# Kernel tuning notes

Measured on AMD Instinct MI355X. Metric: run time of the kernel, lower is better.

## Reference

```python
import jax, jax.numpy as jnp
import numpy as np

B, C, H, W = 8, 128, 256, 256

def setup_inputs() -> dict:
    key = jax.random.key(0)
    k1, k2 = jax.random.split(key)
    inp = jax.random.normal(k1, (B, C, H, W), dtype=jnp.float32)
    # learned per-channel convection vector (kaiming-uniform-ish small values)
    c = jax.random.normal(k2, (C, 2), dtype=jnp.float32) * 2.0
    return {"input": inp, "c": c}

def reference(input, c):
    """Per-channel translation (convection) of a [B,C,H,W] grid by vector c[ch] = (cy, cx),
    via separable bilinear interpolation with zero padding outside the domain:
    out[b,ch,h,w] = input_interp[b, ch, h - c[ch,0], w - c[ch,1]].
    """
    Bs, Cs, Hs, Ws = input.shape

    # ---- interpolate along H ----
    pos_y = jnp.arange(Hs, dtype=c.dtype)[None, :] - c[:, 0][:, None]   # [C,H]
    y0f = jnp.floor(pos_y)
    wy = pos_y - y0f                                                     # frac weight [C,H]
    y0 = y0f.astype(jnp.int32)
    y1 = y0 + 1

    def gather_h(idx):  # idx [C,H] -> [B,C,H,W], zero outside
        valid = ((idx >= 0) & (idx < Hs)).astype(input.dtype)
        idxc = jnp.clip(idx, 0, Hs - 1)
        g = jnp.take_along_axis(input, idxc[None, :, :, None], axis=2)
        return g * valid[None, :, :, None]

    xh = gather_h(y0) * (1.0 - wy)[None, :, :, None] + gather_h(y1) * wy[None, :, :, None]

    # ---- interpolate along W ----
    pos_x = jnp.arange(Ws, dtype=c.dtype)[None, :] - c[:, 1][:, None]   # [C,W]
    x0f = jnp.floor(pos_x)
    wx = pos_x - x0f                                                     # [C,W]
    x0 = x0f.astype(jnp.int32)
    x1 = x0 + 1

    def gather_w(idx):  # idx [C,W] -> [B,C,H,W], zero outside
        valid = ((idx >= 0) & (idx < Ws)).astype(input.dtype)
        idxc = jnp.clip(idx, 0, Ws - 1)
        g = jnp.take_along_axis(xh, idxc[None, :, None, :], axis=3)
        return g * valid[None, :, None, :]

    out = gather_w(x0) * (1.0 - wx)[None, :, None, :] + gather_w(x1) * wx[None, :, None, :]
    return out
```

## Files before the change

### kernel.cpp

```cpp
#include <hip/hip_runtime.h>

constexpr int Cn = 128, Hn = 256, Wn = 256;

__global__ __launch_bounds__(256) void convection_kernel(
    const float* __restrict__ in, const float* __restrict__ cvec, float* __restrict__ out)
{
    const int lane  = threadIdx.x & 63;
    const int wave  = (int)blockIdx.x * 4 + (threadIdx.x >> 6);
    const int plane = wave >> 3;
    const int h0    = (wave & 7) << 5;
    const int ch    = plane & (Cn - 1);

    const float cy = cvec[2 * ch];
    const float cx = cvec[2 * ch + 1];
    const float* __restrict__ pin = in  + ((long long)plane << 16);
    float* __restrict__ pout      = out + ((long long)plane << 16);

    const float ncx = fminf(fmaxf(-cx, -600.f), 600.f);
    const int D = (int)floorf(ncx);
    const int s = D >> 2;
    const int r = D & 3;
    int q0 = lane + s;     q0 = q0 < 0 ? 0 : (q0 > 63 ? 63 : q0);
    int q1 = lane + s + 1; q1 = q1 < 0 ? 0 : (q1 > 63 ? 63 : q1);

    float fx0[4], fx1[4];
    #pragma unroll
    for (int j = 0; j < 4; ++j) {
        const int   col  = 4 * lane + j;
        const float posx = (float)col - cx;
        const int   e0   = col + D;
        const float wx   = posx - (float)e0;
        fx0[j] = ((unsigned)e0       < (unsigned)Wn) ? (1.0f - wx) : 0.0f;
        fx1[j] = ((unsigned)(e0 + 1) < (unsigned)Wn) ? wx          : 0.0f;
    }

    auto mkwin = [&](const float4 g, float* w) {
        const float u0 = __shfl(g.x, q0), u1 = __shfl(g.y, q0),
                    u2 = __shfl(g.z, q0), u3 = __shfl(g.w, q0);
        const float u4 = __shfl(g.x, q1), u5 = __shfl(g.y, q1),
                    u6 = __shfl(g.z, q1), u7 = __shfl(g.w, q1);
        switch (r) {
            case 0:  w[0]=u0; w[1]=u1; w[2]=u2; w[3]=u3; w[4]=u4; break;
            case 1:  w[0]=u1; w[1]=u2; w[2]=u3; w[3]=u4; w[4]=u5; break;
            case 2:  w[0]=u2; w[1]=u3; w[2]=u4; w[3]=u5; w[4]=u6; break;
            default: w[0]=u3; w[1]=u4; w[2]=u5; w[3]=u6; w[4]=u7; break;
        }
    };
    auto y0of = [&](int h) -> int {
        const float p = (float)h - cy;
        const float f = floorf(p);
        return (int)fminf(fmaxf(f, -600.f), 600.f);
    };

    int y0c = y0of(h0);
    const int rA = min(max(y0c,     0), 255);
    const int rB = min(max(y0c + 1, 0), 255);
    const float4 A = *(const float4*)(pin + (rA << 8) + 4 * lane);
    const float4 B = *(const float4*)(pin + (rB << 8) + 4 * lane);
    float w0[5], w1[5], wn[5];
    mkwin(A, w0); mkwin(B, w1);

    for (int h = h0; h < h0 + 32; ++h) {
        const int y0n = y0of(h + 1);
        const int rG  = min(max(y0n + 1, 0), 255);
        const float4 G = *(const float4*)(pin + (rG << 8) + 4 * lane);

        const float posy = (float)h - cy;
        const float wy   = posy - (float)y0c;
        const float f0   = ((unsigned)y0c       < (unsigned)Hn) ? (1.0f - wy) : 0.0f;
        const float f1   = ((unsigned)(y0c + 1) < (unsigned)Hn) ? wy          : 0.0f;
        const float xh0 = f0*w0[0] + f1*w1[0];
        const float xh1 = f0*w0[1] + f1*w1[1];
        const float xh2 = f0*w0[2] + f1*w1[2];
        const float xh3 = f0*w0[3] + f1*w1[3];
        const float xh4 = f0*w0[4] + f1*w1[4];
        float4 o;
        o.x = fx0[0]*xh0 + fx1[0]*xh1;
        o.y = fx0[1]*xh1 + fx1[1]*xh2;
        o.z = fx0[2]*xh2 + fx1[2]*xh3;
        o.w = fx0[3]*xh3 + fx1[3]*xh4;
        *(float4*)(pout + (h << 8) + 4 * lane) = o;

        const int dk = __builtin_amdgcn_readfirstlane(y0n - y0c);
        if (dk == 1) {
            mkwin(G, wn);
            #pragma unroll
            for (int i = 0; i < 5; ++i) { w0[i] = w1[i]; w1[i] = wn[i]; }
        } else if (dk != 0) {
            const int rN = min(max(y0n, 0), 255);
            const float4 N = *(const float4*)(pin + (rN << 8) + 4 * lane);
            mkwin(N, w0);
            mkwin(G, w1);
        }
        y0c = y0n;
    }
}

extern "C" void kernel_launch(void* const* d_in, const int* in_sizes, int n_in,
                              void* d_out, int out_size, void* d_ws, size_t ws_size,
                              hipStream_t stream) {
    const float* in = (const float*)d_in[0];
    const float* c  = (const float*)d_in[1];
    float* out      = (float*)d_out;

    dim3 block(256);
    dim3 grid(2048);
    hipLaunchKernelGGL(convection_kernel, grid, block, 0, stream, in, c, out);
}
```

Baseline: 441.2 us.

## Batch row loads in groups of eight to expose memory-level parallelism

Restructures the per-row streaming loop into groups of 8 output rows. When the source rows in a group advance one per output row (the common case for a constant per-channel shift), it issues all 9 needed row loads up front, builds the shuffle windows, then computes 8 outputs fully unrolled. This breaks the serial load-use dependency of the rolling window so more loads are in flight per wave. The cost is higher register pressure from 9 float4s and 45 window values, and a slower fallback path that reloads two rows per output row.

After: 436.1 us. Within noise of the previous version (-1.2%).

```diff
diff --git a/kernel.cpp b/kernel.cpp
--- a/kernel.cpp
+++ b/kernel.cpp
@@ -34,7 +34,7 @@
         fx1[j] = ((unsigned)(e0 + 1) < (unsigned)Wn) ? wx          : 0.0f;
     }
 
-    auto mkwin = [&](const float4 g, float* w) {
+    auto mkwin = [&](const float4 g, float (&w)[5]) {
         const float u0 = __shfl(g.x, q0), u1 = __shfl(g.y, q0),
                     u2 = __shfl(g.z, q0), u3 = __shfl(g.w, q0);
         const float u4 = __shfl(g.x, q1), u5 = __shfl(g.y, q1),
@@ -51,48 +51,71 @@
         const float f = floorf(p);
         return (int)fminf(fmaxf(f, -600.f), 600.f);
     };
+    auto clampRow = [](int v) -> int { return v < 0 ? 0 : (v > Hn - 1 ? Hn - 1 : v); };
 
-    int y0c = y0of(h0);
-    const int rA = min(max(y0c,     0), 255);
-    const int rB = min(max(y0c + 1, 0), 255);
-    const float4 A = *(const float4*)(pin + (rA << 8) + 4 * lane);
-    const float4 B = *(const float4*)(pin + (rB << 8) + 4 * lane);
-    float w0[5], w1[5], wn[5];
-    mkwin(A, w0); mkwin(B, w1);
+    for (int g = 0; g < 4; ++g) {
+        const int hg  = h0 + 8 * g;
+        const int y00 = y0of(hg);
 
-    for (int h = h0; h < h0 + 32; ++h) {
-        const int y0n = y0of(h + 1);
-        const int rG  = min(max(y0n + 1, 0), 255);
-        const float4 G = *(const float4*)(pin + (rG << 8) + 4 * lane);
+        bool mono = true;
+        #pragma unroll
+        for (int j = 1; j < 8; ++j) mono = mono && (y0of(hg + j) == y00 + j);
 
-        const float posy = (float)h - cy;
-        const float wy   = posy - (float)y0c;
-        const float f0   = ((unsigned)y0c       < (unsigned)Hn) ? (1.0f - wy) : 0.0f;
-        const float f1   = ((unsigned)(y0c + 1) < (unsigned)Hn) ? wy          : 0.0f;
-        const float xh0 = f0*w0[0] + f1*w1[0];
-        const float xh1 = f0*w0[1] + f1*w1[1];
-        const float xh2 = f0*w0[2] + f1*w1[2];
-        const float xh3 = f0*w0[3] + f1*w1[3];
-        const float xh4 = f0*w0[4] + f1*w1[4];
-        float4 o;
-        o.x = fx0[0]*xh0 + fx1[0]*xh1;
-        o.y = fx0[1]*xh1 + fx1[1]*xh2;
-        o.z = fx0[2]*xh2 + fx1[2]*xh3;
-        o.w = fx0[3]*xh3 + fx1[3]*xh4;
-        *(float4*)(pout + (h << 8) + 4 * lane) = o;
+        if (mono) {
+            float4 R[9];
+            #pragma unroll
+            for (int i = 0; i < 9; ++i)
+                R[i] = *(const float4*)(pin + (clampRow(y00 + i) << 8) + 4 * lane);
 
-        const int dk = __builtin_amdgcn_readfirstlane(y0n - y0c);
-        if (dk == 1) {
-            mkwin(G, wn);
+            float W[9][5];
             #pragma unroll
-            for (int i = 0; i < 5; ++i) { w0[i] = w1[i]; w1[i] = wn[i]; }
-        } else if (dk != 0) {
-            const int rN = min(max(y0n, 0), 255);
-            const float4 N = *(const float4*)(pin + (rN << 8) + 4 * lane);
-            mkwin(N, w0);
-            mkwin(G, w1);
+            for (int i = 0; i < 9; ++i) mkwin(R[i], W[i]);
+
+            #pragma unroll
+            for (int j = 0; j < 8; ++j) {
+                const int   h    = hg + j;
+                const int   y0   = y00 + j;
+                const float posy = (float)h - cy;
+                const float wy   = posy - (float)y0;
+                const float f0   = ((unsigned)y0       < (unsigned)Hn) ? (1.0f - wy) : 0.0f;
+                const float f1   = ((unsigned)(y0 + 1) < (unsigned)Hn) ? wy          : 0.0f;
+                const float xh0 = f0*W[j][0] + f1*W[j+1][0];
+                const float xh1 = f0*W[j][1] + f1*W[j+1][1];
+                const float xh2 = f0*W[j][2] + f1*W[j+1][2];
+                const float xh3 = f0*W[j][3] + f1*W[j+1][3];
+                const float xh4 = f0*W[j][4] + f1*W[j+1][4];
+                float4 o;
+                o.x = fx0[0]*xh0 + fx1[0]*xh1;
+                o.y = fx0[1]*xh1 + fx1[1]*xh2;
+                o.z = fx0[2]*xh2 + fx1[2]*xh3;
+                o.w = fx0[3]*xh3 + fx1[3]*xh4;
+                *(float4*)(pout + (h << 8) + 4 * lane) = o;
+            }
+        } else {
+            for (int j = 0; j < 8; ++j) {
+                const int   h    = hg + j;
+                const int   y0   = y0of(h);
+                const float posy = (float)h - cy;
+                const float wy   = posy - (float)y0;
+                const float f0   = ((unsigned)y0       < (unsigned)Hn) ? (1.0f - wy) : 0.0f;
+                const float f1   = ((unsigned)(y0 + 1) < (unsigned)Hn) ? wy          : 0.0f;
+                const float4 Ra = *(const float4*)(pin + (clampRow(y0)     << 8) + 4 * lane);
+                const float4 Rb = *(const float4*)(pin + (clampRow(y0 + 1) << 8) + 4 * lane);
+                float wa[5], wb[5];
+                mkwin(Ra, wa); mkwin(Rb, wb);
+                const float xh0 = f0*wa[0] + f1*wb[0];
+                const float xh1 = f0*wa[1] + f1*wb[1];
+                const float xh2 = f0*wa[2] + f1*wb[2];
+                const float xh3 = f0*wa[3] + f1*wb[3];
+                const float xh4 = f0*wa[4] + f1*wb[4];
+                float4 o;
+                o.x = fx0[0]*xh0 + fx1[0]*xh1;
+                o.y = fx0[1]*xh1 + fx1[1]*xh2;
+                o.z = fx0[2]*xh2 + fx1[2]*xh3;
+                o.w = fx0[3]*xh3 + fx1[3]*xh4;
+                *(float4*)(pout + (h << 8) + 4 * lane) = o;
+            }
         }
-        y0c = y0n;
     }
 }
 
```
